# Kernel optimization log

Measured on AMD Instinct MI355X. Metric: run time of the kernel, lower is better.

Reference implementation:

```python
import jax, jax.numpy as jnp
import numpy as np

IMAGE_SIZE = 64                 # Rasterize(image_size=64, anti_aliasing=True)
RASTER = IMAGE_SIZE * 2 * 2     # init doubles for AA, forward doubles again -> 256
CHUNK = 64
B, NV, NF = 4, 1024, 1024


def setup_inputs() -> dict:
    key = jax.random.key(0)
    k1, k2 = jax.random.split(key)
    vertices = jax.random.uniform(k1, (B, NV, 2), dtype=jnp.float32, minval=-1.0, maxval=1.0)
    faces = jax.random.randint(k2, (B, NF, 3), 0, NV, dtype=jnp.int32)
    return {"vertices": vertices, "faces": faces}


def _pixel_grid(s):
    # NMR-style pixel centers in NDC: p = (2i + 1 - s) / s
    c = (2.0 * jnp.arange(s, dtype=jnp.float32) + 1.0 - s) / s
    py, px = jnp.meshgrid(c, c, indexing="ij")
    return px.reshape(-1), py.reshape(-1)  # (P,), (P,)


def _hard_raster(face_xy, s):
    # face_xy: (B, Nf, 3, 2). Coverage = any face whose 3 edge cross products are all > 0.
    # Faces are duplicated with reversed winding upstream, so a one-sided test covers
    # every non-degenerate triangle regardless of orientation.
    px, py = _pixel_grid(s)
    b, nft = face_xy.shape[:2]
    chunks = face_xy.reshape(b, nft // CHUNK, CHUNK, 3, 2).transpose(1, 0, 2, 3, 4)

    def step(cov, fc):
        v = fc                              # (B, C, 3, 2)
        vn = jnp.roll(v, -1, axis=2)        # next vertex per edge
        ex = (vn[..., 0] - v[..., 0])[..., None]   # (B, C, 3, 1)
        ey = (vn[..., 1] - v[..., 1])[..., None]
        cross = ex * (py - v[..., 1][..., None]) - ey * (px - v[..., 0][..., None])  # (B,C,3,P)
        inside = jnp.all(cross > 0, axis=2)        # (B, C, P)
        return jnp.logical_or(cov, jnp.any(inside, axis=1)), None

    cov0 = jnp.zeros((b, s * s), dtype=bool)
    cov, _ = jax.lax.scan(step, cov0, chunks)
    return cov.astype(jnp.float32).reshape(b, s, s)


def reference(vertices, faces):
    # forward: double faces with reversed winding, gather vertex coords per face
    faces2 = jnp.concatenate([faces, faces[:, :, ::-1]], axis=1)         # (B, 2Nf, 3)
    face_xy = jax.vmap(lambda v, f: v[f])(vertices, faces2)              # (B, 2Nf, 3, 2)
    alpha = _hard_raster(face_xy, RASTER)                                # (B, RASTER, RASTER)
    alpha = alpha[:, ::-1, :]                                            # vertical flip
    b, s, _ = alpha.shape
    alpha = alpha.reshape(b, s // 2, 2, s // 2, 2).mean(axis=(2, 4))     # avg_pool2d k=2
    return alpha
```

## Files before the change

kernel.cpp:

```cpp
#include <hip/hip_runtime.h>


constexpr int S     = 256;
constexpr int NVERT = 1024;
constexpr int NFACE = 1024;
constexpr int OUTSZ = 128;

__global__ __launch_bounds__(256)
void raster_fused(const float* __restrict__ verts,
                  const int*   __restrict__ faces,
                  float*       __restrict__ out)
{
    __shared__ float2 vlds[NVERT];
    __shared__ unsigned long long covMask;

    const int b    = blockIdx.z;
    const int tid  = threadIdx.x;
    const int lane = tid & 63;
    const int wid  = tid >> 6;
    const int tx   = lane & 7;
    const int ty   = lane >> 3;
    const int bx   = (int)(blockIdx.x << 3);
    const int by   = (int)(blockIdx.y << 3);
    const int sx   = bx + tx;
    const int sy   = by + ty;

    const float px  = (float)(2 * sx + 1 - S)       * (1.0f / (float)S);
    const float py  = (float)(2 * sy + 1 - S)       * (1.0f / (float)S);
    const float rx0 = (float)(2 * bx + 1 - S)       * (1.0f / (float)S);
    const float rx1 = (float)(2 * (bx + 7) + 1 - S) * (1.0f / (float)S);
    const float ry0 = (float)(2 * by + 1 - S)       * (1.0f / (float)S);
    const float ry1 = (float)(2 * (by + 7) + 1 - S) * (1.0f / (float)S);
    constexpr float MARGIN = 1e-4f;
    const float cx = (rx0 + rx1) * 0.5f;
    const float cy = (ry0 + ry1) * 0.5f;
    const float h  = (rx1 - rx0) * 0.5f;
    const float rx0m = rx0 - MARGIN, rx1m = rx1 + MARGIN;
    const float ry0m = ry0 - MARGIN, ry1m = ry1 + MARGIN;

    {
        const float4* __restrict__ v4 = (const float4*)(verts + (size_t)b * NVERT * 2);
        float4* __restrict__ l4 = (float4*)vlds;
        #pragma unroll
        for (int i = 0; i < NVERT / 2 / 256; ++i)
            l4[tid + i * 256] = v4[tid + i * 256];
    }
    if (tid == 0) covMask = 0ull;
    __syncthreads();

    const int* __restrict__ fb = faces + (size_t)b * NFACE * 3;

    bool covered = false;

    int c0 = wid * 64;
    int i0 = fb[3 * (c0 + lane) + 0];
    int i1 = fb[3 * (c0 + lane) + 1];
    int i2 = fb[3 * (c0 + lane) + 2];

    for (; c0 < NFACE; c0 += 256) {
        const int nc = c0 + 256;
        int n0 = 0, n1 = 0, n2 = 0;
        if (nc < NFACE) {
            n0 = fb[3 * (nc + lane) + 0];
            n1 = fb[3 * (nc + lane) + 1];
            n2 = fb[3 * (nc + lane) + 2];
        }

        const float2 va = vlds[i0], vbb = vlds[i1], vcc = vlds[i2];
        const float xa = va.x,  ya = va.y;
        const float xb = vbb.x, yb = vbb.y;
        const float xc = vcc.x, yc = vcc.y;
        const float exab = __fsub_rn(xb, xa), eyab = __fsub_rn(yb, ya);
        const float exbc = __fsub_rn(xc, xb), eybc = __fsub_rn(yc, yb);
        const float exca = __fsub_rn(xa, xc), eyca = __fsub_rn(ya, yc);

        bool keep;
        {
            const float xmn = fminf(xa, fminf(xb, xc));
            const float xmx = fmaxf(xa, fmaxf(xb, xc));
            const float ymn = fminf(ya, fminf(yb, yc));
            const float ymx = fmaxf(ya, fmaxf(yb, yc));
            const bool bbok = (xmn <= rx1m) & (xmx >= rx0m) &
                              (ymn <= ry1m) & (ymx >= ry0m);
            #define EDGE_CR(ex, ey, vx, vy, Fc, rr)                           \
                const float Fc = (ex) * (cy - (vy)) - (ey) * (cx - (vx));     \
                const float rr = (fabsf(ex) + fabsf(ey)) * h;
            EDGE_CR(exab, eyab, xa, ya, FcAB, rAB)
            EDGE_CR(exbc, eybc, xb, yb, FcBC, rBC)
            EDGE_CR(exca, eyca, xc, yc, FcCA, rCA)
            #undef EDGE_CR
            const bool fwdP = (FcAB + rAB > -MARGIN) & (FcBC + rBC > -MARGIN) &
                              (FcCA + rCA > -MARGIN);
            const bool revP = (FcAB - rAB <  MARGIN) & (FcBC - rBC <  MARGIN) &
                              (FcCA - rCA <  MARGIN);
            keep = bbok & (fwdP | revP);
        }

        unsigned long long m = __ballot((int)keep);
        int nt = 0;
        #define RL(v) __int_as_float(__builtin_amdgcn_readlane(__float_as_int(v), f))
        while (m) {
            const int f = __ffsll(m) - 1;
            m &= m - 1;
            const float Xa = RL(xa), Ya = RL(ya);
            const float Xb = RL(xb), Yb = RL(yb);
            const float Xc = RL(xc), Yc = RL(yc);
            const float E0x = RL(exab), E0y = RL(eyab);
            const float E1x = RL(exbc), E1y = RL(eybc);
            const float E2x = RL(exca), E2y = RL(eyca);
            const float dxa = __fsub_rn(px, Xa), dya = __fsub_rn(py, Ya);
            const float dxb = __fsub_rn(px, Xb), dyb = __fsub_rn(py, Yb);
            const float dxc = __fsub_rn(px, Xc), dyc = __fsub_rn(py, Yc);
            const float F0 = __fsub_rn(__fmul_rn(E0x, dya), __fmul_rn(E0y, dxa));
            const float F1 = __fsub_rn(__fmul_rn(E1x, dyb), __fmul_rn(E1y, dxb));
            const float F2 = __fsub_rn(__fmul_rn(E2x, dyc), __fmul_rn(E2y, dxc));
            const float R0 = __fsub_rn(__fmul_rn(E1y, dxc), __fmul_rn(E1x, dyc));
            const float R1 = __fsub_rn(__fmul_rn(E0y, dxb), __fmul_rn(E0x, dyb));
            const float R2 = __fsub_rn(__fmul_rn(E2y, dxa), __fmul_rn(E2x, dya));
            const bool fwd = (F0 > 0.0f) & (F1 > 0.0f) & (F2 > 0.0f);
            const bool rev = (R0 > 0.0f) & (R1 > 0.0f) & (R2 > 0.0f);
            covered = covered || fwd || rev;
            if (((++nt) & 3) == 0 && __all((int)covered)) break;
        }
        #undef RL

        const unsigned long long m2 = __ballot((int)covered);
        unsigned long long u = 0ull;
        if (lane == 0) u = atomicOr(&covMask, m2) | m2;
        u = __shfl(u, 0);
        if (u == ~0ull) break;

        i0 = n0; i1 = n1; i2 = n2;
    }

    __syncthreads();

    if (tid < 64) {
        const unsigned long long u = covMask;
        if (((tx & 1) == 0) && ((ty & 1) == 0)) {
            const float c = (float)(((u >> lane) & 1ull) +
                                    ((u >> (lane ^ 1)) & 1ull) +
                                    ((u >> (lane ^ 8)) & 1ull) +
                                    ((u >> (lane ^ 9)) & 1ull));
            const int X = sx >> 1;
            const int Y = (OUTSZ - 1) - (sy >> 1);
            out[((size_t)b * OUTSZ + Y) * OUTSZ + X] = c * 0.25f;
        }
    }
}

extern "C" void kernel_launch(void* const* d_in, const int* in_sizes, int n_in,
                              void* d_out, int out_size, void* d_ws, size_t ws_size,
                              hipStream_t stream) {
    const float* verts = (const float*)d_in[0];
    const int*   faces = (const int*)d_in[1];
    float*       out   = (float*)d_out;

    const int B = in_sizes[0] / (NVERT * 2);
    dim3 grid(S / 8, S / 8, B);
    raster_fused<<<grid, dim3(256), 0, stream>>>(verts, faces, out);
}
```

Before: 19.55 us.

## Assign one 8x8 tile per wavefront instead of splitting faces across waves

Each wavefront now owns its own 8x8 pixel tile and walks all faces, so a block covers four tiles rather than four waves sharing one tile's face list. This removes the shared-memory atomicOr coverage mask, the second block barrier and the LDS readback, and lets each wave exit early on its own once every pixel is covered. The 2x2 average pool now uses wave shuffles. In exchange, each wave does a serial walk over the full face list with no split across waves, and the grid has a quarter as many blocks, so vertex loading into LDS is amortized over four tiles.

```diff
diff --git a/kernel.cpp b/kernel.cpp
--- a/kernel.cpp
+++ b/kernel.cpp
@@ -7,21 +7,22 @@
 constexpr int OUTSZ = 128;
 
 __global__ __launch_bounds__(256)
-void raster_fused(const float* __restrict__ verts,
-                  const int*   __restrict__ faces,
-                  float*       __restrict__ out)
+void raster_wpt(const float* __restrict__ verts,
+                const int*   __restrict__ faces,
+                float*       __restrict__ out)
 {
     __shared__ float2 vlds[NVERT];
-    __shared__ unsigned long long covMask;
 
-    const int b    = blockIdx.z;
     const int tid  = threadIdx.x;
     const int lane = tid & 63;
     const int wid  = tid >> 6;
+    const int t    = (int)blockIdx.x * 4 + wid;
+    const int b    = t >> 10;
+    const int tt   = t & 1023;
+    const int bx   = (tt & 31) << 3;
+    const int by   = (tt >> 5) << 3;
     const int tx   = lane & 7;
     const int ty   = lane >> 3;
-    const int bx   = (int)(blockIdx.x << 3);
-    const int by   = (int)(blockIdx.y << 3);
     const int sx   = bx + tx;
     const int sy   = by + ty;
 
@@ -41,24 +42,21 @@
     {
         const float4* __restrict__ v4 = (const float4*)(verts + (size_t)b * NVERT * 2);
         float4* __restrict__ l4 = (float4*)vlds;
-        #pragma unroll
-        for (int i = 0; i < NVERT / 2 / 256; ++i)
-            l4[tid + i * 256] = v4[tid + i * 256];
+        l4[tid]       = v4[tid];
+        l4[tid + 256] = v4[tid + 256];
     }
-    if (tid == 0) covMask = 0ull;
     __syncthreads();
 
     const int* __restrict__ fb = faces + (size_t)b * NFACE * 3;
 
     bool covered = false;
 
-    int c0 = wid * 64;
-    int i0 = fb[3 * (c0 + lane) + 0];
-    int i1 = fb[3 * (c0 + lane) + 1];
-    int i2 = fb[3 * (c0 + lane) + 2];
+    int i0 = fb[3 * lane + 0];
+    int i1 = fb[3 * lane + 1];
+    int i2 = fb[3 * lane + 2];
 
-    for (; c0 < NFACE; c0 += 256) {
-        const int nc = c0 + 256;
+    for (int c0 = 0; c0 < NFACE; c0 += 64) {
+        const int nc = c0 + 64;
         int n0 = 0, n1 = 0, n2 = 0;
         if (nc < NFACE) {
             n0 = fb[3 * (nc + lane) + 0];
@@ -124,28 +122,17 @@
         }
         #undef RL
 
-        const unsigned long long m2 = __ballot((int)covered);
-        unsigned long long u = 0ull;
-        if (lane == 0) u = atomicOr(&covMask, m2) | m2;
-        u = __shfl(u, 0);
-        if (u == ~0ull) break;
-
+        if (__all((int)covered)) break;
         i0 = n0; i1 = n1; i2 = n2;
     }
 
-    __syncthreads();
-
-    if (tid < 64) {
-        const unsigned long long u = covMask;
-        if (((tx & 1) == 0) && ((ty & 1) == 0)) {
-            const float c = (float)(((u >> lane) & 1ull) +
-                                    ((u >> (lane ^ 1)) & 1ull) +
-                                    ((u >> (lane ^ 8)) & 1ull) +
-                                    ((u >> (lane ^ 9)) & 1ull));
-            const int X = sx >> 1;
-            const int Y = (OUTSZ - 1) - (sy >> 1);
-            out[((size_t)b * OUTSZ + Y) * OUTSZ + X] = c * 0.25f;
-        }
+    float c = covered ? 1.0f : 0.0f;
+    c += __shfl_xor(c, 1);
+    c += __shfl_xor(c, 8);
+    if (((lane & 1) == 0) && ((lane & 8) == 0)) {
+        const int X = sx >> 1;
+        const int Y = (OUTSZ - 1) - (sy >> 1);
+        out[((size_t)b * OUTSZ + Y) * OUTSZ + X] = c * 0.25f;
     }
 }
 
@@ -157,6 +144,6 @@
     float*       out   = (float*)d_out;
 
     const int B = in_sizes[0] / (NVERT * 2);
-    dim3 grid(S / 8, S / 8, B);
-    raster_fused<<<grid, dim3(256), 0, stream>>>(verts, faces, out);
+    const int nTiles = B * (S / 8) * (S / 8);
+    raster_wpt<<<dim3(nTiles / 4), dim3(256), 0, stream>>>(verts, faces, out);
 }
```

New measurement: 20.77 us. 6.2% more time.
